# Optimization experiments

Measured on AMD Instinct MI355X. Metric: run time of the kernel, lower is better.

## Reference

```python
import jax, jax.numpy as jnp
import numpy as np

# Architecture constants (from init_kwargs)
A, L, NCF = 200, 10, 9            # num_agent, in_len, num_control_features
D_MODEL, N_HEADS = 1024, 4
HEAD_DIM = D_MODEL // N_HEADS      # 256 (the module's 'head_dim')
PER_HEAD = HEAD_DIM // N_HEADS     # 64 (effective per-head dim after rearrange)
SCALE = HEAD_DIM ** -0.5           # module scales by head_dim**-0.5
N = A * L + NCF                    # 2009 tokens


def _build_mask():
    # block-diagonal agent mask: eye(A) repeat_interleaved L on both axes,
    # then zero-padded by NCF rows/cols for control features
    m = np.kron(np.eye(A, dtype=np.float32), np.ones((L, L), dtype=np.float32))
    m = np.pad(m, ((0, NCF), (0, NCF)))
    return jnp.asarray(m)  # [N, N]

_MASK = _build_mask()


def setup_inputs() -> dict:
    key = jax.random.key(0)
    k0, k1, k2, k3 = jax.random.split(key, 4)
    x = jax.random.normal(k0, (4, N, D_MODEL), jnp.float32)
    W_qkv = jax.random.normal(k1, (D_MODEL, HEAD_DIM * 3), jnp.float32) * 0.02
    W_qk_self = jax.random.normal(k2, (D_MODEL, HEAD_DIM * 2), jnp.float32) * 0.02
    W_out = jax.random.normal(k3, (HEAD_DIM, D_MODEL), jnp.float32) * 0.02
    b_out = jnp.zeros((D_MODEL,), jnp.float32)
    return {"x": x, "W_qkv": W_qkv, "W_qk_self": W_qk_self,
            "W_out": W_out, "b_out": b_out}


def _heads(t, b, n):
    # 'b n (h d) -> b h n d' with h = N_HEADS
    return t.reshape(b, n, N_HEADS, PER_HEAD).transpose(0, 2, 1, 3)


def reference(x, W_qkv, W_qk_self, W_out, b_out):
    b, n, _ = x.shape
    q, k, v = jnp.split(x @ W_qkv, 3, axis=-1)          # each [b, n, HEAD_DIM]
    q, k, v = _heads(q, b, n), _heads(k, b, n), _heads(v, b, n)  # [b,h,n,d]
    q_self, k_self = jnp.split(x @ W_qk_self, 2, axis=-1)
    q_self, k_self = _heads(q_self, b, n), _heads(k_self, b, n)

    dots = jnp.einsum('bhnd,bhmd->bhnm', q, k) * SCALE
    dots_self = jnp.einsum('bhnd,bhmd->bhnm', q_self, k_self) * SCALE
    dots_all = _MASK * dots_self + (1.0 - _MASK) * dots  # blend via block mask
    attn = jax.nn.softmax(dots_all, axis=-1)             # [b,h,n,n]

    out = jnp.einsum('bhnm,bhmd->bhnd', attn, v)
    out = out.transpose(0, 2, 1, 3).reshape(b, n, HEAD_DIM)  # 'b h n d -> b n (h d)'
    out = out @ W_out + b_out                            # to_out (dropout=0)
    return out, attn
```

## Files before the change

### kernel.cpp

```cpp
#include <hip/hip_runtime.h>

typedef unsigned short u16;
typedef unsigned int u32;
typedef short short8 __attribute__((ext_vector_type(8)));
typedef float f32x4 __attribute__((ext_vector_type(4)));
typedef float f32x16 __attribute__((ext_vector_type(16)));
typedef float float4a __attribute__((ext_vector_type(4), aligned(4)));

#define NTOK 2009
#define M8   8036
#define DMOD 1024
#define PKBH 129024

static __device__ __forceinline__ u16 f2bf(float f) {
  unsigned int x = __float_as_uint(f);
  x += 0x7fffu + ((x >> 16) & 1u);
  return (u16)(x >> 16);
}
static __device__ __forceinline__ float bf2f(u16 u) {
  return __uint_as_float((unsigned int)u << 16);
}
static __device__ __forceinline__ u32 pk2(float a, float b) {
  return (u32)f2bf(a) | ((u32)f2bf(b) << 16);
}
static __device__ __forceinline__ u32 cvtpk(float a, float b) {
  u32 d;
  asm("v_cvt_pk_bf16_f32 %0, %1, %2" : "=v"(d) : "v"(a), "v"(b));
  return d;
}
static __device__ __forceinline__ void gload_lds16(const void* g, void* l) {
  __builtin_amdgcn_global_load_lds(
      (const __attribute__((address_space(1))) void*)g,
      (__attribute__((address_space(3))) void*)l, 16, 0, 0);
}

__global__ void k_convs(const float* __restrict__ x, u16* __restrict__ xb,
                        const float* __restrict__ Wqkv, const float* __restrict__ Wqs,
                        u16* __restrict__ WtCat,
                        const float* __restrict__ Wout, u16* __restrict__ WtOut) {
  int blk = blockIdx.x;
  if (blk < 8036) {
    int i = blk * 256 + threadIdx.x;
    float4 v = ((const float4*)x)[i];
    unsigned int a = (unsigned int)f2bf(v.x) | ((unsigned int)f2bf(v.y) << 16);
    unsigned int b = (unsigned int)f2bf(v.z) | ((unsigned int)f2bf(v.w) << 16);
    ((uint2*)xb)[i] = make_uint2(a, b);
  } else if (blk < 8036 + 5120) {
    int i = (blk - 8036) * 256 + threadIdx.x;
    int n = i >> 10, k = i & 1023;
    float v = (n < 768) ? Wqkv[k * 768 + n] : Wqs[k * 512 + (n - 768)];
    WtCat[i] = f2bf(v);
  } else {
    int i = (blk - 8036 - 5120) * 256 + threadIdx.x;
    int n = i >> 8, k = i & 255;
    WtOut[i] = f2bf(Wout[k * 1024 + n]);
  }
}

__global__ __launch_bounds__(256) void k_gemm_proj(
    const u16* __restrict__ A, const u16* __restrict__ Bt,
    u16* __restrict__ Qp, u16* __restrict__ Kp, u16* __restrict__ Vp,
    u16* __restrict__ Qsb, u16* __restrict__ Ksb)
{
  __shared__ u16 Asm[128 * 64];
  __shared__ u16 Bsm[128 * 64];
  int mt = blockIdx.x * 128, nt = blockIdx.y * 128;
  int tid = threadIdx.x, lane = tid & 63, w = tid >> 6;
  int wm = w >> 1, wn = w & 1;
  int fr = lane & 15, fq = lane >> 4;
  int srow = w * 32 + (lane >> 3);
  int scol = (lane & 7) * 8;
  f32x4 acc[4][4];
#pragma unroll
  for (int a = 0; a < 4; ++a)
#pragma unroll
    for (int b = 0; b < 4; ++b) acc[a][b] = (f32x4){0.f, 0.f, 0.f, 0.f};

  for (int kt = 0; kt < 1024; kt += 64) {
#pragma unroll
    for (int j = 0; j < 4; ++j) {
      int r = srow + j * 8;
      int am = mt + r; if (am >= M8) am = 0;
      gload_lds16(A + (size_t)am * 1024 + kt + scol, Asm + (size_t)(w * 32 + j * 8) * 64);
      gload_lds16(Bt + (size_t)(nt + r) * 1024 + kt + scol, Bsm + (size_t)(w * 32 + j * 8) * 64);
    }
    __syncthreads();
#pragma unroll
    for (int cs = 0; cs < 2; ++cs) {
      short8 af[4], bf[4];
#pragma unroll
      for (int i = 0; i < 4; ++i) {
        af[i] = *(const short8*)&Asm[(size_t)(wm * 64 + i * 16 + fr) * 64 + cs * 32 + fq * 8];
        bf[i] = *(const short8*)&Bsm[(size_t)(wn * 64 + i * 16 + fr) * 64 + cs * 32 + fq * 8];
      }
#pragma unroll
      for (int mi = 0; mi < 4; ++mi)
#pragma unroll
        for (int ni = 0; ni < 4; ++ni)
          acc[mi][ni] = __builtin_amdgcn_mfma_f32_16x16x32_bf16(af[mi], bf[ni], acc[mi][ni], 0, 0, 0);
    }
    __syncthreads();
  }

#pragma unroll
  for (int ni = 0; ni < 4; ++ni) {
    int n = nt + wn * 64 + ni * 16 + fr;
    int g = n >> 6, d = n & 63;
    int h = g & 3, sel = g >> 2;
    float scl = (sel == 0 || sel == 3) ? 0.0625f : 1.0f;
#pragma unroll
    for (int mi = 0; mi < 4; ++mi) {
#pragma unroll
      for (int i = 0; i < 4; ++i) {
        int m = mt + wm * 64 + mi * 16 + fq * 4 + i;
        if (m >= M8) continue;
        int b_ = m / NTOK, tok = m - b_ * NTOK;
        int bh = b_ * 4 + h;
        u16 val = f2bf(acc[mi][ni][i] * scl);
        if (sel <= 1) {
          u16* dst = sel == 0 ? Qp : Kp;
          size_t idx = ((((size_t)bh * 63 + (tok >> 5)) * 4 + (d >> 4)) * 2 + ((d >> 3) & 1)) * 256
                       + (tok & 31) * 8 + (d & 7);
          dst[idx] = val;
        } else if (sel == 2) {
          size_t idx = (((((size_t)bh * 63 + (tok >> 5)) * 2 + (d >> 5)) * 2 + ((tok >> 4) & 1)) * 2
                        + ((tok >> 3) & 1)) * 256 + (d & 31) * 8 + (tok & 7);
          Vp[idx] = val;
        } else {
          u16* p = (sel == 3) ? Qsb : Ksb;
          p[((size_t)bh * NTOK + tok) * 64 + d] = val;
        }
      }
    }
  }
}

__global__ void k_self(const u16* __restrict__ Qs, const u16* __restrict__ Ks,
                       float* __restrict__ selfS) {
  int blk = blockIdx.x;
  int bh = blk / 200, a = blk % 200;
  int t = threadIdx.x;
  if (t >= 100) return;
  int ri = t / 10, rj = t % 10;
  const u16* qp = &Qs[((size_t)bh * NTOK + a * 10 + ri) * 64];
  const u16* kp = &Ks[((size_t)bh * NTOK + a * 10 + rj) * 64];
  float s = 0.f;
#pragma unroll 8
  for (int k = 0; k < 64; ++k) s += bf2f(qp[k]) * bf2f(kp[k]);
  selfS[(size_t)blk * 100 + t] = s;
}

__global__ __launch_bounds__(256, 2) void k_attn13(
    const u16* __restrict__ Qp, const u16* __restrict__ Kp,
    const u16* __restrict__ Vp, const float* __restrict__ selfS,
    float* __restrict__ attn, u16* __restrict__ Ob)
{
  __shared__ float s_sum[4][32];
  __shared__ float s_o[4][64][32];
  int bh = blockIdx.x;
  int qt = blockIdx.y;
  int q0 = qt * 32;
  int tid = threadIdx.x;
  int lane = tid & 63, w = tid >> 6;
  int ql = lane & 31, h = lane >> 5;
  int qg = q0 + ql;
  bool qok = qg < NTOK;
  int qc = qok ? qg : NTOK - 1;
  int lo8 = ql * 8;

  const u16* qbase = Qp + (size_t)bh * PKBH + (size_t)qt * 2048;
  const u16* kbase = Kp + (size_t)bh * PKBH;
  const u16* vbase = Vp + (size_t)bh * PKBH;

  short8 qf[4];
#pragma unroll
  for (int c = 0; c < 4; ++c)
    qf[c] = *(const short8*)&qbase[(c * 2 + h) * 256 + lo8];

  int qa = (qg < 2000) ? (qg / 10) : -1;
  int band_lo = 1 << 30, band_hi = -(1 << 30);
  if (q0 < 2000) {
    int hi_row = (q0 + 31 < 1999) ? q0 + 31 : 1999;
    band_lo = (q0 / 10) * 10;
    band_hi = (hi_row / 10) * 10 + 10;
  }
  const float* sfb = &selfS[(size_t)bh * 20000];

  int t0 = w * 16;
  int t1 = t0 + 16; if (t1 > 63) t1 = 63;

  u32 pb[16][8];
  short8 kf[4], kfn[4], vf[4];
  f32x16 oacc0 = {}, oacc1 = {};

#pragma unroll
  for (int c = 0; c < 4; ++c)
    kf[c] = *(const short8*)&kbase[(size_t)t0 * 2048 + (c * 2 + h) * 256 + lo8];
  float ssum = 0.f;
#pragma unroll
  for (int i = 0; i < 16; ++i) {
    int t = t0 + i;
    if (t < t1) {
      int tn = (t + 1 < t1) ? t + 1 : t0;
#pragma unroll
      for (int c = 0; c < 4; ++c)
        vf[c] = *(const short8*)&vbase[(size_t)t * 2048 + (c * 2 + h) * 256 + lo8];
#pragma unroll
      for (int c = 0; c < 4; ++c)
        kfn[c] = *(const short8*)&kbase[(size_t)tn * 2048 + (c * 2 + h) * 256 + lo8];
      f32x16 acc = {};
#pragma unroll
      for (int c = 0; c < 4; ++c)
        acc = __builtin_amdgcn_mfma_f32_32x32x16_bf16(kf[c], qf[c], acc, 0, 0, 0);
      int kt = t * 32;
      float e[16];
      if ((kt < band_hi) && (kt + 32 > band_lo)) {
#pragma unroll
        for (int r = 0; r < 16; ++r) {
          int kc = kt + (r & 3) + 8 * (r >> 2) + 4 * h;
          float sc = acc[r];
          if (qa >= 0 && kc < 2000 && (kc / 10) == qa)
            sc = sfb[qa * 100 + (qg - qa * 10) * 10 + (kc - qa * 10)];
          e[r] = __expf(sc);
        }
      } else {
#pragma unroll
        for (int r = 0; r < 16; ++r) e[r] = __expf(acc[r]);
      }
      if (t == 62) {
#pragma unroll
        for (int r = 0; r < 16; ++r) {
          int kc = kt + (r & 3) + 8 * (r >> 2) + 4 * h;
          if (kc >= NTOK) e[r] = 0.f;
        }
      }
#pragma unroll
      for (int r2 = 0; r2 < 8; ++r2) {
        pb[i][r2] = cvtpk(e[2 * r2], e[2 * r2 + 1]);
        ssum += e[2 * r2] + e[2 * r2 + 1];
      }
      u32 p00 = __shfl_xor(pb[i][0], 32), p01 = __shfl_xor(pb[i][1], 32);
      u32 p10 = __shfl_xor(pb[i][2], 32), p11 = __shfl_xor(pb[i][3], 32);
      u32 p20 = __shfl_xor(pb[i][4], 32), p21 = __shfl_xor(pb[i][5], 32);
      u32 p30 = __shfl_xor(pb[i][6], 32), p31 = __shfl_xor(pb[i][7], 32);
      u32 b0[4], b1[4];
      b0[0] = h ? p10 : pb[i][0];  b0[1] = h ? p11 : pb[i][1];
      b0[2] = h ? pb[i][2] : p00;  b0[3] = h ? pb[i][3] : p01;
      b1[0] = h ? p30 : pb[i][4];  b1[1] = h ? p31 : pb[i][5];
      b1[2] = h ? pb[i][6] : p20;  b1[3] = h ? pb[i][7] : p21;
      short8 B0, B1;
      __builtin_memcpy(&B0, b0, 16);
      __builtin_memcpy(&B1, b1, 16);
      oacc0 = __builtin_amdgcn_mfma_f32_32x32x16_bf16(vf[0], B0, oacc0, 0, 0, 0);
      oacc1 = __builtin_amdgcn_mfma_f32_32x32x16_bf16(vf[2], B0, oacc1, 0, 0, 0);
      oacc0 = __builtin_amdgcn_mfma_f32_32x32x16_bf16(vf[1], B1, oacc0, 0, 0, 0);
      oacc1 = __builtin_amdgcn_mfma_f32_32x32x16_bf16(vf[3], B1, oacc1, 0, 0, 0);
#pragma unroll
      for (int c = 0; c < 4; ++c) kf[c] = kfn[c];
    }
  }
  ssum += __shfl_xor(ssum, 32);
  if (lane < 32) s_sum[w][ql] = ssum;
  __syncthreads();
  float inv = 1.0f / (s_sum[0][ql] + s_sum[1][ql] + s_sum[2][ql] + s_sum[3][ql]);

  float* arow = &attn[((size_t)bh * NTOK + qc) * NTOK];
#pragma unroll
  for (int i = 0; i < 16; ++i) {
    int t = t0 + i;
    if (t < t1 && qok) {
      int kt = t * 32;
      float e[16];
#pragma unroll
      for (int r2 = 0; r2 < 8; ++r2) {
        u32 u = pb[i][r2];
        e[2 * r2]     = __uint_as_float(u << 16) * inv;
        e[2 * r2 + 1] = __uint_as_float(u & 0xffff0000u) * inv;
      }
      if (t < 62) {
#pragma unroll
        for (int rq = 0; rq < 4; ++rq) {
          int col0 = kt + 8 * rq + 4 * h;
          *(float4a*)&arow[col0] =
              (float4a){e[4 * rq], e[4 * rq + 1], e[4 * rq + 2], e[4 * rq + 3]};
        }
      } else {
#pragma unroll
        for (int rq = 0; rq < 4; ++rq) {
          int col0 = kt + 8 * rq + 4 * h;
          if (col0 + 3 < NTOK) {
            *(float4a*)&arow[col0] =
                (float4a){e[4 * rq], e[4 * rq + 1], e[4 * rq + 2], e[4 * rq + 3]};
          } else {
#pragma unroll
            for (int j = 0; j < 4; ++j)
              if (col0 + j < NTOK) arow[col0 + j] = e[4 * rq + j];
          }
        }
      }
    }
  }

#pragma unroll
  for (int r = 0; r < 16; ++r) {
    int d = (r & 3) + 8 * (r >> 2) + 4 * h;
    s_o[w][d][ql] = oacc0[r];
    s_o[w][d + 32][ql] = oacc1[r];
  }
  __syncthreads();
  {
    int q = tid & 31, dg = tid >> 5;
    int qg2 = q0 + q;
    if (qg2 < NTOK) {
      float invq = 1.0f / (s_sum[0][q] + s_sum[1][q] + s_sum[2][q] + s_sum[3][q]);
      int b_ = bh >> 2, hd = bh & 3;
      u16* orow = &Ob[((size_t)(b_ * NTOK + qg2)) * 256 + hd * 64 + dg * 8];
      u32 wpk[4];
#pragma unroll
      for (int j = 0; j < 4; ++j) {
        int d = dg * 8 + 2 * j;
        float a = (s_o[0][d][q] + s_o[1][d][q] + s_o[2][d][q] + s_o[3][d][q]) * invq;
        float b = (s_o[0][d + 1][q] + s_o[1][d + 1][q] + s_o[2][d + 1][q] + s_o[3][d + 1][q]) * invq;
        wpk[j] = pk2(a, b);
      }
      *(uint4*)orow = make_uint4(wpk[0], wpk[1], wpk[2], wpk[3]);
    }
  }
}

__global__ __launch_bounds__(256) void k_gemm_out(
    const u16* __restrict__ A, const u16* __restrict__ Bt,
    const float* __restrict__ bias, float* __restrict__ C)
{
  __shared__ u16 Asm[128 * 64];
  __shared__ u16 Bsm[128 * 64];
  int mt = blockIdx.x * 128, nt = blockIdx.y * 128;
  int tid = threadIdx.x, lane = tid & 63, w = tid >> 6;
  int wm = w >> 1, wn = w & 1;
  int fr = lane & 15, fq = lane >> 4;
  int srow = w * 32 + (lane >> 3);
  int scol = (lane & 7) * 8;
  f32x4 acc[4][4];
#pragma unroll
  for (int a = 0; a < 4; ++a)
#pragma unroll
    for (int b = 0; b < 4; ++b) acc[a][b] = (f32x4){0.f, 0.f, 0.f, 0.f};

  for (int kt = 0; kt < 256; kt += 64) {
#pragma unroll
    for (int j = 0; j < 4; ++j) {
      int r = srow + j * 8;
      int am = mt + r; if (am >= M8) am = 0;
      gload_lds16(A + (size_t)am * 256 + kt + scol, Asm + (size_t)(w * 32 + j * 8) * 64);
      gload_lds16(Bt + (size_t)(nt + r) * 256 + kt + scol, Bsm + (size_t)(w * 32 + j * 8) * 64);
    }
    __syncthreads();
#pragma unroll
    for (int cs = 0; cs < 2; ++cs) {
      short8 af[4], bf[4];
#pragma unroll
      for (int i = 0; i < 4; ++i) {
        af[i] = *(const short8*)&Asm[(size_t)(wm * 64 + i * 16 + fr) * 64 + cs * 32 + fq * 8];
        bf[i] = *(const short8*)&Bsm[(size_t)(wn * 64 + i * 16 + fr) * 64 + cs * 32 + fq * 8];
      }
#pragma unroll
      for (int mi = 0; mi < 4; ++mi)
#pragma unroll
        for (int ni = 0; ni < 4; ++ni)
          acc[mi][ni] = __builtin_amdgcn_mfma_f32_16x16x32_bf16(af[mi], bf[ni], acc[mi][ni], 0, 0, 0);
    }
    __syncthreads();
  }

#pragma unroll
  for (int ni = 0; ni < 4; ++ni) {
    int n = nt + wn * 64 + ni * 16 + fr;
    float bn = bias[n];
#pragma unroll
    for (int mi = 0; mi < 4; ++mi)
#pragma unroll
      for (int i = 0; i < 4; ++i) {
        int m = mt + wm * 64 + mi * 16 + fq * 4 + i;
        if (m < M8) C[(size_t)m * DMOD + n] = acc[mi][ni][i] + bn;
      }
  }
}

extern "C" void kernel_launch(void* const* d_in, const int* in_sizes, int n_in,
                              void* d_out, int out_size, void* d_ws, size_t ws_size,
                              hipStream_t stream) {
  (void)in_sizes; (void)n_in; (void)out_size; (void)ws_size;
  const float* x    = (const float*)d_in[0];
  const float* Wqkv = (const float*)d_in[1];
  const float* Wqs  = (const float*)d_in[2];
  const float* Wout = (const float*)d_in[3];
  const float* bout = (const float*)d_in[4];
  float* out  = (float*)d_out;
  float* attn = out + (size_t)M8 * DMOD;

  char* ws = (char*)d_ws;
  u16*   xb    = (u16*)(ws);
  u16*   WtCat = (u16*)(ws + 16457728);
  u16*   WtOut = (u16*)(ws + 19079168);
  u16*   Qp    = (u16*)(ws + 19603456);
  u16*   Kp    = (u16*)(ws + 23732224);
  u16*   Vp    = (u16*)(ws + 27860992);
  u16*   Qsb   = (u16*)(ws + 31989760);
  u16*   Ksb   = (u16*)(ws + 36104192);
  u16*   Ob    = (u16*)(ws + 40218624);
  float* selfS = (float*)(ws + 44333056);

  k_convs<<<dim3(8036 + 5120 + 1024), dim3(256), 0, stream>>>(
      x, xb, Wqkv, Wqs, WtCat, Wout, WtOut);
  k_gemm_proj<<<dim3(63, 10), dim3(256), 0, stream>>>(xb, WtCat, Qp, Kp, Vp, Qsb, Ksb);
  k_self<<<dim3(3200), dim3(128), 0, stream>>>(Qsb, Ksb, selfS);
  k_attn13<<<dim3(16, 63), dim3(256), 0, stream>>>(Qp, Kp, Vp, selfS, attn, Ob);
  k_gemm_out<<<dim3(63, 8), dim3(256), 0, stream>>>(Ob, WtOut, bout, out);
}
```

Before: 197.0 us.

## Pad token rows per batch and stage projection epilogue through LDS for vector stores

The bf16 copy of x is padded to 2016 tokens per batch, so each 128-row GEMM tile lies within one batch and 32-token tiles line up. The projection epilogue then writes the accumulator tile into swizzled shared memory (transposed for V) and issues 16-byte vector stores into the packed Q/K/V and self layouts, replacing scattered 2-byte stores that each needed a per-element division. The self-score kernel also loads 8 bf16 values at a time. This adds an extra LDS round trip and barrier, plus some wasted work on the padded rows.

```diff
diff --git a/kernel.cpp b/kernel.cpp
--- a/kernel.cpp
+++ b/kernel.cpp
@@ -9,6 +9,8 @@
 
 #define NTOK 2009
 #define M8   8036
+#define TOKP 2016
+#define M8P  8064
 #define DMOD 1024
 #define PKBH 129024
 
@@ -39,19 +41,25 @@
                         u16* __restrict__ WtCat,
                         const float* __restrict__ Wout, u16* __restrict__ WtOut) {
   int blk = blockIdx.x;
-  if (blk < 8036) {
+  if (blk < 8064) {
     int i = blk * 256 + threadIdx.x;
-    float4 v = ((const float4*)x)[i];
-    unsigned int a = (unsigned int)f2bf(v.x) | ((unsigned int)f2bf(v.y) << 16);
-    unsigned int b = (unsigned int)f2bf(v.z) | ((unsigned int)f2bf(v.w) << 16);
-    ((uint2*)xb)[i] = make_uint2(a, b);
-  } else if (blk < 8036 + 5120) {
-    int i = (blk - 8036) * 256 + threadIdx.x;
+    int b = i / (TOKP * 256);
+    int rem = i - b * (TOKP * 256);
+    int tok = rem >> 8, dg = rem & 255;
+    uint2 o = make_uint2(0u, 0u);
+    if (tok < NTOK) {
+      float4 v = ((const float4*)x)[(size_t)(b * NTOK + tok) * 256 + dg];
+      o.x = (u32)f2bf(v.x) | ((u32)f2bf(v.y) << 16);
+      o.y = (u32)f2bf(v.z) | ((u32)f2bf(v.w) << 16);
+    }
+    ((uint2*)xb)[i] = o;
+  } else if (blk < 8064 + 5120) {
+    int i = (blk - 8064) * 256 + threadIdx.x;
     int n = i >> 10, k = i & 1023;
     float v = (n < 768) ? Wqkv[k * 768 + n] : Wqs[k * 512 + (n - 768)];
     WtCat[i] = f2bf(v);
   } else {
-    int i = (blk - 8036 - 5120) * 256 + threadIdx.x;
+    int i = (blk - 8064 - 5120) * 256 + threadIdx.x;
     int n = i >> 8, k = i & 255;
     WtOut[i] = f2bf(Wout[k * 1024 + n]);
   }
@@ -62,8 +70,9 @@
     u16* __restrict__ Qp, u16* __restrict__ Kp, u16* __restrict__ Vp,
     u16* __restrict__ Qsb, u16* __restrict__ Ksb)
 {
-  __shared__ u16 Asm[128 * 64];
-  __shared__ u16 Bsm[128 * 64];
+  __shared__ u16 smem[2][128 * 64];
+  u16* Asm = smem[0];
+  u16* Bsm = smem[1];
   int mt = blockIdx.x * 128, nt = blockIdx.y * 128;
   int tid = threadIdx.x, lane = tid & 63, w = tid >> 6;
   int wm = w >> 1, wn = w & 1;
@@ -80,8 +89,7 @@
 #pragma unroll
     for (int j = 0; j < 4; ++j) {
       int r = srow + j * 8;
-      int am = mt + r; if (am >= M8) am = 0;
-      gload_lds16(A + (size_t)am * 1024 + kt + scol, Asm + (size_t)(w * 32 + j * 8) * 64);
+      gload_lds16(A + (size_t)(mt + r) * 1024 + kt + scol, Asm + (size_t)(w * 32 + j * 8) * 64);
       gload_lds16(Bt + (size_t)(nt + r) * 1024 + kt + scol, Bsm + (size_t)(w * 32 + j * 8) * 64);
     }
     __syncthreads();
@@ -102,33 +110,61 @@
     __syncthreads();
   }
 
+  int sel = nt >> 8;
+  float scl = (sel == 0 || sel == 3) ? 0.0625f : 1.0f;
+  bool T = (sel == 2);
+  u16* Csm = smem[0];
 #pragma unroll
   for (int ni = 0; ni < 4; ++ni) {
-    int n = nt + wn * 64 + ni * 16 + fr;
-    int g = n >> 6, d = n & 63;
-    int h = g & 3, sel = g >> 2;
-    float scl = (sel == 0 || sel == 3) ? 0.0625f : 1.0f;
 #pragma unroll
     for (int mi = 0; mi < 4; ++mi) {
 #pragma unroll
       for (int i = 0; i < 4; ++i) {
-        int m = mt + wm * 64 + mi * 16 + fq * 4 + i;
-        if (m >= M8) continue;
-        int b_ = m / NTOK, tok = m - b_ * NTOK;
-        int bh = b_ * 4 + h;
+        int rm = wm * 64 + mi * 16 + fq * 4 + i;
+        int cn = wn * 64 + ni * 16 + fr;
         u16 val = f2bf(acc[mi][ni][i] * scl);
-        if (sel <= 1) {
-          u16* dst = sel == 0 ? Qp : Kp;
-          size_t idx = ((((size_t)bh * 63 + (tok >> 5)) * 4 + (d >> 4)) * 2 + ((d >> 3) & 1)) * 256
-                       + (tok & 31) * 8 + (d & 7);
-          dst[idx] = val;
-        } else if (sel == 2) {
-          size_t idx = (((((size_t)bh * 63 + (tok >> 5)) * 2 + (d >> 5)) * 2 + ((tok >> 4) & 1)) * 2
-                        + ((tok >> 3) & 1)) * 256 + (d & 31) * 8 + (tok & 7);
-          Vp[idx] = val;
-        } else {
-          u16* p = (sel == 3) ? Qsb : Ksb;
-          p[((size_t)bh * NTOK + tok) * 64 + d] = val;
+        if (!T) Csm[rm * 128 + (cn ^ ((rm & 7) << 3))] = val;
+        else    Csm[cn * 128 + (rm ^ ((cn & 7) << 3))] = val;
+      }
+    }
+  }
+  __syncthreads();
+
+  int t = tid;
+#pragma unroll
+  for (int rg = 0; rg < 4; ++rg) {
+    int row_g = mt + rg * 32;
+    int b_ = row_g / TOKP;
+    int tok0 = row_g - b_ * TOKP;
+    int tile = tok0 >> 5;
+#pragma unroll
+    for (int g2 = 0; g2 < 2; ++g2) {
+      int g = ((nt + g2 * 64) >> 6);
+      int h = g & 3;
+      int bh = b_ * 4 + h;
+      int Lrow, Lcol0;
+      if (sel <= 1) {
+        Lrow = rg * 32 + (t & 31);
+        Lcol0 = g2 * 64 + (t >> 5) * 8;
+        short8 v = *(const short8*)&Csm[Lrow * 128 + (Lcol0 ^ ((Lrow & 7) << 3))];
+        u16* dst = (sel == 0 ? Qp : Kp) + ((size_t)bh * 63 + tile) * 2048
+                   + (t >> 5) * 256 + (t & 31) * 8;
+        *(short8*)dst = v;
+      } else if (sel == 2) {
+        Lrow = g2 * 64 + (t >> 7) * 32 + (t & 31);
+        Lcol0 = rg * 32 + ((t >> 5) & 3) * 8;
+        short8 v = *(const short8*)&Csm[Lrow * 128 + (Lcol0 ^ ((Lrow & 7) << 3))];
+        u16* dst = Vp + ((size_t)bh * 63 + tile) * 2048 + (t >> 5) * 256 + (t & 31) * 8;
+        *(short8*)dst = v;
+      } else {
+        int tok_l = t >> 3;
+        int tok_g = tok0 + tok_l;
+        if (tok_g < NTOK) {
+          Lrow = rg * 32 + tok_l;
+          Lcol0 = g2 * 64 + (t & 7) * 8;
+          short8 v = *(const short8*)&Csm[Lrow * 128 + (Lcol0 ^ ((Lrow & 7) << 3))];
+          u16* dst = (sel == 3 ? Qsb : Ksb) + ((size_t)bh * NTOK + tok_g) * 64 + (t & 7) * 8;
+          *(short8*)dst = v;
         }
       }
     }
@@ -142,11 +178,15 @@
   int t = threadIdx.x;
   if (t >= 100) return;
   int ri = t / 10, rj = t % 10;
-  const u16* qp = &Qs[((size_t)bh * NTOK + a * 10 + ri) * 64];
-  const u16* kp = &Ks[((size_t)bh * NTOK + a * 10 + rj) * 64];
+  const short8* qv = (const short8*)&Qs[((size_t)bh * NTOK + a * 10 + ri) * 64];
+  const short8* kv = (const short8*)&Ks[((size_t)bh * NTOK + a * 10 + rj) * 64];
   float s = 0.f;
-#pragma unroll 8
-  for (int k = 0; k < 64; ++k) s += bf2f(qp[k]) * bf2f(kp[k]);
+#pragma unroll
+  for (int c = 0; c < 8; ++c) {
+    short8 qa = qv[c], kb = kv[c];
+#pragma unroll
+    for (int j = 0; j < 8; ++j) s += bf2f((u16)qa[j]) * bf2f((u16)kb[j]);
+  }
   selfS[(size_t)blk * 100 + t] = s;
 }
 
@@ -400,17 +440,17 @@
 
   char* ws = (char*)d_ws;
   u16*   xb    = (u16*)(ws);
-  u16*   WtCat = (u16*)(ws + 16457728);
-  u16*   WtOut = (u16*)(ws + 19079168);
-  u16*   Qp    = (u16*)(ws + 19603456);
-  u16*   Kp    = (u16*)(ws + 23732224);
-  u16*   Vp    = (u16*)(ws + 27860992);
-  u16*   Qsb   = (u16*)(ws + 31989760);
-  u16*   Ksb   = (u16*)(ws + 36104192);
-  u16*   Ob    = (u16*)(ws + 40218624);
-  float* selfS = (float*)(ws + 44333056);
-
-  k_convs<<<dim3(8036 + 5120 + 1024), dim3(256), 0, stream>>>(
+  u16*   WtCat = (u16*)(ws + 16515072);
+  u16*   WtOut = (u16*)(ws + 19136512);
+  u16*   Qp    = (u16*)(ws + 19660800);
+  u16*   Kp    = (u16*)(ws + 23789568);
+  u16*   Vp    = (u16*)(ws + 27918336);
+  u16*   Qsb   = (u16*)(ws + 32047104);
+  u16*   Ksb   = (u16*)(ws + 36161536);
+  u16*   Ob    = (u16*)(ws + 40275968);
+  float* selfS = (float*)(ws + 44390400);
+
+  k_convs<<<dim3(8064 + 5120 + 1024), dim3(256), 0, stream>>>(
       x, xb, Wqkv, Wqs, WtCat, Wout, WtOut);
   k_gemm_proj<<<dim3(63, 10), dim3(256), 0, stream>>>(xb, WtCat, Qp, Kp, Vp, Qsb, Ksb);
   k_self<<<dim3(3200), dim3(128), 0, stream>>>(Qsb, Ksb, selfS);
```

Measured after the change: 187.2 us. 5.0% less time.
